# Kernel optimization log

Measured on AMD Instinct MI355X. Metric: run time of the kernel, lower is better.

## Reference

```python
import jax, jax.numpy as jnp
import numpy as np

D = 128
EPS = 1e-5

def group_norm1(x, gamma, beta):
    # GroupNorm with num_groups=1 over channel dim of [N, C]
    mu = jnp.mean(x, axis=-1, keepdims=True)
    var = jnp.mean(jnp.square(x - mu), axis=-1, keepdims=True)
    xhat = (x - mu) * jax.lax.rsqrt(var + EPS)
    return xhat * gamma + beta

def setup_inputs() -> dict:
    key = jax.random.key(0)
    ks = jax.random.split(key, 12)
    N_ctx, N_tgt, E = 40000, 40000, 640000
    s = 0.09  # ~1/sqrt(128) weight scale
    inp = {
        'context_feat': jax.random.normal(ks[0], (N_ctx, D), jnp.float32),
        'target_feat': jax.random.normal(ks[1], (N_tgt, D), jnp.float32),
        'context_pose': jax.random.normal(ks[2], (N_ctx, 4), jnp.float32),
        'target_pose': jax.random.normal(ks[3], (N_tgt, 4), jnp.float32),
        'W_input': s * jax.random.normal(ks[4], (D, D), jnp.float32),
        'W_rp': 0.5 * jax.random.normal(ks[5], (4, D), jnp.float32),
        'b_rp': jnp.zeros((D,), jnp.float32),
        'W_c1': s * jax.random.normal(ks[6], (2 * D, D), jnp.float32),
        'g_c1': jnp.ones((D,), jnp.float32),
        'b_c1': jnp.zeros((D,), jnp.float32),
        'W_c2': s * jax.random.normal(ks[7], (D, D), jnp.float32),
        'g_n': jnp.ones((D,), jnp.float32),
        'b_n': jnp.zeros((D,), jnp.float32),
        'W_m1': s * jax.random.normal(ks[8], (D, D), jnp.float32),
        'g_m1': jnp.ones((D,), jnp.float32),
        'bm1': jnp.zeros((D,), jnp.float32),
        'W_m2': s * jax.random.normal(ks[9], (D, D), jnp.float32),
        'g_m2': jnp.ones((D,), jnp.float32),
        'bm2': jnp.zeros((D,), jnp.float32),
        'hi': jax.random.randint(ks[10], (E,), 0, N_ctx, jnp.int32),
        'wi': jax.random.randint(ks[11], (E,), 0, N_tgt, jnp.int32),
    }
    return inp

def reference(context_feat, target_feat, context_pose, target_pose,
              W_input, W_rp, b_rp, W_c1, g_c1, b_c1, W_c2,
              g_n, b_n, W_m1, g_m1, bm1, W_m2, g_m2, bm2, hi, wi):
    # relpose: Linear(4,128) + ReLU on relative pose of each (context, target) edge
    dist_feat = context_pose[hi] - target_pose[wi]                 # [E, 4]
    dist_feat = jax.nn.relu(dist_feat @ W_rp + b_rp)               # [E, 128]
    # ctx: Linear(256,128,GN,ReLU) -> Linear(128,128, no bias)
    ctx = jnp.concatenate([context_feat[hi], dist_feat], axis=-1)  # [E, 256]
    ctx = jax.nn.relu(group_norm1(ctx @ W_c1, g_c1, b_c1))
    ctx = ctx @ W_c2                                               # [E, 128]
    # input linear + index_add scatter into targets
    tf = target_feat @ W_input                                     # [N_tgt, 128]
    tf = tf + jax.ops.segment_sum(ctx, wi, num_segments=target_feat.shape[0])
    tf = jax.nn.relu(group_norm1(tf, g_n, b_n))
    # mlp: Linear(GN,ReLU) -> Linear(GN, no act)
    tf = jax.nn.relu(group_norm1(tf @ W_m1, g_m1, bm1))
    tf = group_norm1(tf @ W_m2, g_m2, bm2)
    # residual + relu
    return jax.nn.relu(tf + target_feat)
```

## Files before the change

kernel.cpp:

```cpp
#include <hip/hip_runtime.h>

#define D 128
#define EPSV 1e-5f

typedef __attribute__((ext_vector_type(8))) __bf16 bf16x8;
typedef __attribute__((ext_vector_type(4))) float f32x4;

__device__ __forceinline__ ushort f2bf(float x) {
  unsigned u = __float_as_uint(x);
  u += 0x7fffu + ((u >> 16) & 1u);
  return (ushort)(u >> 16);
}
__device__ __forceinline__ unsigned cvtpk(float lo, float hi) {
  unsigned r;
  asm("v_cvt_pk_bf16_f32 %0, %1, %2" : "=v"(r) : "v"(lo), "v"(hi));
  return r;
}
__device__ __forceinline__ int yidx(int row, int col) {
  return row * 128 + (col ^ ((row & 7) << 3));
}

__global__ void k_cvt(const float* __restrict__ Wc1, const float* __restrict__ Wc2,
                      ushort* __restrict__ WT1, ushort* __restrict__ WT2) {
  int i = blockIdx.x * 256 + threadIdx.x;
  if (i < 128 * 256) {
    int n = i >> 8, k = i & 255;
    WT1[i] = f2bf(Wc1[k * 128 + n]);
  } else {
    int j = i - 128 * 256;
    if (j < 128 * 128) {
      int n = j >> 7, k = j & 127;
      WT2[j] = f2bf(Wc2[k * 128 + n]);
    }
  }
}

__global__ void k_cvtf(const float* __restrict__ cf, ushort* __restrict__ cb,
                       int n8) {
  int i = blockIdx.x * 256 + threadIdx.x;
  if (i < n8) {
    float4 f0 = *(const float4*)(cf + (size_t)i * 8);
    float4 f1 = *(const float4*)(cf + (size_t)i * 8 + 4);
    uint4 p;
    p.x = cvtpk(f0.x, f0.y); p.y = cvtpk(f0.z, f0.w);
    p.z = cvtpk(f1.x, f1.y); p.w = cvtpk(f1.z, f1.w);
    *(uint4*)(cb + (size_t)i * 8) = p;
  }
}

template <bool BF16CF>
__global__ __launch_bounds__(256, 3) void k_edge(
    const float* __restrict__ cfeat, const ushort* __restrict__ cfb,
    const float* __restrict__ cpose, const float* __restrict__ tpose,
    const float* __restrict__ Wrp, const float* __restrict__ brp,
    const float* __restrict__ gc1, const float* __restrict__ bc1,
    const ushort* __restrict__ WT1, const ushort* __restrict__ WT2,
    const int* __restrict__ hi, const int* __restrict__ wi,
    float* __restrict__ acc, int E) {
  __shared__ ushort Wbuf[2][4096];
  __shared__ ushort Ybuf[128 * 128];
  __shared__ float gnbuf[2][128][2];
  __shared__ int wl[128];

  const int t = threadIdx.x;
  const int lane = t & 63;
  const int wv = t >> 6;
  const int wm = wv >> 1, wn = wv & 1;
  const int s = lane & 15, g = lane >> 4;
  const int e0 = blockIdx.x * 128;

  auto stage = [&](int c, int nb) {
    const ushort* Wt = (c < 8) ? WT1 : WT2;
    const int koff = (c < 8 ? c : c - 8) * 32;
    const int krow = (c < 8) ? 256 : 128;
    const int col = t & 127, g0 = t >> 7;
#pragma unroll
    for (int v = 0; v < 2; ++v) {
      const int gg = g0 + v * 2;
      const ushort* src = Wt + (size_t)col * krow + koff + gg * 8;
      ushort* dst = &Wbuf[nb][(gg * 128 + col) * 8];
      __builtin_amdgcn_global_load_lds(
          (const __attribute__((address_space(1))) void*)src,
          (__attribute__((address_space(3))) void*)dst, 16, 0, 0);
    }
  };

  stage(0, 0);
  if (t < 128) wl[t] = wi[min(e0 + t, E - 1)];

  int hl[4];
#pragma unroll
  for (int m = 0; m < 4; ++m)
    hl[m] = hi[min(e0 + wm * 64 + m * 16 + s, E - 1)];

  bf16x8 cf01[2][4];
  if (BF16CF) {
#pragma unroll
    for (int kc = 0; kc < 2; ++kc)
#pragma unroll
      for (int m = 0; m < 4; ++m)
        cf01[kc][m] =
            *(const bf16x8*)(cfb + (size_t)hl[m] * D + kc * 32 + g * 8);
  }

  {
    const int e = t >> 1;
    const int jh = (t & 1) * 64;
    const int ge = min(e0 + e, E - 1);
    const int h = hi[ge], w = wi[ge];
    float4 cp = *(const float4*)(cpose + (size_t)h * 4);
    float4 tp = *(const float4*)(tpose + (size_t)w * 4);
    const float d0 = cp.x - tp.x, d1 = cp.y - tp.y;
    const float d2 = cp.z - tp.z, d3 = cp.w - tp.w;
#pragma unroll
    for (int q = 0; q < 16; ++q) {
      const int j = jh + q * 4;
      float4 b  = *(const float4*)(brp + j);
      float4 w0 = *(const float4*)(Wrp + j);
      float4 w1 = *(const float4*)(Wrp + D + j);
      float4 w2 = *(const float4*)(Wrp + 2 * D + j);
      float4 w3 = *(const float4*)(Wrp + 3 * D + j);
      float r0 = fmaxf(b.x + d0 * w0.x + d1 * w1.x + d2 * w2.x + d3 * w3.x, 0.f);
      float r1 = fmaxf(b.y + d0 * w0.y + d1 * w1.y + d2 * w2.y + d3 * w3.y, 0.f);
      float r2 = fmaxf(b.z + d0 * w0.z + d1 * w1.z + d2 * w2.z + d3 * w3.z, 0.f);
      float r3 = fmaxf(b.w + d0 * w0.w + d1 * w1.w + d2 * w2.w + d3 * w3.w, 0.f);
      *(uint2*)&Ybuf[yidx(e, j)] = make_uint2(cvtpk(r0, r1), cvtpk(r2, r3));
    }
  }
  __syncthreads();

  f32x4 acc1[4][4];
#pragma unroll
  for (int m = 0; m < 4; ++m)
#pragma unroll
    for (int n = 0; n < 4; ++n) acc1[m][n] = (f32x4){0.f, 0.f, 0.f, 0.f};

  for (int kc = 0; kc < 8; ++kc) {
    const int nb = kc & 1;
    stage(kc + 1, nb ^ 1);
    bf16x8 a[4];
    if (kc < 4) {
      if (BF16CF) {
        if (kc < 2) {
#pragma unroll
          for (int m = 0; m < 4; ++m) a[m] = cf01[kc][m];
        } else {
#pragma unroll
          for (int m = 0; m < 4; ++m)
            a[m] = *(const bf16x8*)(cfb + (size_t)hl[m] * D + kc * 32 + g * 8);
        }
      } else {
#pragma unroll
        for (int m = 0; m < 4; ++m) {
          const float* src = cfeat + (size_t)hl[m] * D + kc * 32 + g * 8;
          float4 f0 = *(const float4*)src;
          float4 f1 = *(const float4*)(src + 4);
          union { uint4 u; bf16x8 v; } cv;
          cv.u.x = cvtpk(f0.x, f0.y); cv.u.y = cvtpk(f0.z, f0.w);
          cv.u.z = cvtpk(f1.x, f1.y); cv.u.w = cvtpk(f1.z, f1.w);
          a[m] = cv.v;
        }
      }
    } else {
#pragma unroll
      for (int m = 0; m < 4; ++m)
        a[m] = *(const bf16x8*)
            &Ybuf[yidx(wm * 64 + m * 16 + s, (kc - 4) * 32 + g * 8)];
    }
#pragma unroll
    for (int n = 0; n < 4; ++n) {
      bf16x8 b = *(const bf16x8*)
          &Wbuf[nb][(g * 128 + wn * 64 + n * 16 + s) * 8];
#pragma unroll
      for (int m = 0; m < 4; ++m)
        acc1[m][n] =
            __builtin_amdgcn_mfma_f32_16x16x32_bf16(a[m], b, acc1[m][n], 0, 0, 0);
    }
    __syncthreads();
  }

#pragma unroll
  for (int m = 0; m < 4; ++m) {
#pragma unroll
    for (int reg = 0; reg < 4; ++reg) {
      float p1 = acc1[m][0][reg] + acc1[m][1][reg] + acc1[m][2][reg] +
                 acc1[m][3][reg];
      float p2 = acc1[m][0][reg] * acc1[m][0][reg] +
                 acc1[m][1][reg] * acc1[m][1][reg] +
                 acc1[m][2][reg] * acc1[m][2][reg] +
                 acc1[m][3][reg] * acc1[m][3][reg];
#pragma unroll
      for (int msk = 1; msk < 16; msk <<= 1) {
        p1 += __shfl_xor(p1, msk, 64);
        p2 += __shfl_xor(p2, msk, 64);
      }
      if (s == 0) {
        const int row = wm * 64 + m * 16 + g * 4 + reg;
        *(float2*)&gnbuf[wn][row][0] = make_float2(p1, p2);
      }
    }
  }
  __syncthreads();

  {
    float gcl[4], bcl[4];
#pragma unroll
    for (int n = 0; n < 4; ++n) {
      gcl[n] = gc1[wn * 64 + n * 16 + s];
      bcl[n] = bc1[wn * 64 + n * 16 + s];
    }
#pragma unroll
    for (int m = 0; m < 4; ++m) {
#pragma unroll
      for (int reg = 0; reg < 4; ++reg) {
        const int row = wm * 64 + m * 16 + g * 4 + reg;
        float2 q0 = *(const float2*)&gnbuf[0][row][0];
        float2 q1 = *(const float2*)&gnbuf[1][row][0];
        const float mean = (q0.x + q1.x) * (1.f / 128.f);
        const float var = (q0.y + q1.y) * (1.f / 128.f) - mean * mean;
        const float rstd = rsqrtf(var + EPSV);
#pragma unroll
        for (int n = 0; n < 4; ++n) {
          float y = fmaxf((acc1[m][n][reg] - mean) * rstd * gcl[n] + bcl[n], 0.f);
          Ybuf[yidx(row, wn * 64 + n * 16 + s)] = (ushort)cvtpk(y, y);
        }
      }
    }
  }
  __syncthreads();

  f32x4 acc2[4][4];
#pragma unroll
  for (int m = 0; m < 4; ++m)
#pragma unroll
    for (int n = 0; n < 4; ++n) acc2[m][n] = (f32x4){0.f, 0.f, 0.f, 0.f};

  for (int kc = 0; kc < 4; ++kc) {
    const int c = 8 + kc;
    const int nb = c & 1;
    if (c < 11) stage(c + 1, nb ^ 1);
    bf16x8 a[4];
#pragma unroll
    for (int m = 0; m < 4; ++m)
      a[m] = *(const bf16x8*)
          &Ybuf[yidx(wm * 64 + m * 16 + s, kc * 32 + g * 8)];
#pragma unroll
    for (int n = 0; n < 4; ++n) {
      bf16x8 b = *(const bf16x8*)
          &Wbuf[nb][(g * 128 + wn * 64 + n * 16 + s) * 8];
#pragma unroll
      for (int m = 0; m < 4; ++m)
        acc2[m][n] =
            __builtin_amdgcn_mfma_f32_16x16x32_bf16(a[m], b, acc2[m][n], 0, 0, 0);
    }
    if (kc < 3) __syncthreads();
  }

#pragma unroll
  for (int m = 0; m < 4; ++m) {
#pragma unroll
    for (int reg = 0; reg < 4; ++reg) {
      const int rl = wm * 64 + m * 16 + g * 4 + reg;
      if (e0 + rl < E) {
        const int w = wl[rl];
        float* base = acc + (size_t)w * D + wn * 64 + s;
#pragma unroll
        for (int n = 0; n < 4; ++n)
          unsafeAtomicAdd(base + n * 16, acc2[m][n][reg]);
      }
    }
  }
}

__device__ __forceinline__ void reduce16(float& a, float& b) {
#pragma unroll
  for (int w = 1; w < 16; w <<= 1) {
    a += __shfl_xor(a, w, 64);
    b += __shfl_xor(b, w, 64);
  }
}

__global__ __launch_bounds__(256, 2) void k_input(
    const float* __restrict__ tfeat, const float* __restrict__ Wi,
    float* __restrict__ acc, int N) {
  __shared__ float Wbuf[64][132];
  __shared__ float xt[64][132];
  const int t = threadIdx.x;
  const int r = t >> 4, s = t & 15, j0 = s * 8;
  const int row0 = blockIdx.x * 64;

  for (int idx = t; idx < 64 * 32; idx += 256) {
    int rr = idx >> 5, c4 = idx & 31;
    int grow = row0 + rr;
    float4 v = make_float4(0.f, 0.f, 0.f, 0.f);
    if (grow < N) v = *(const float4*)(tfeat + (size_t)grow * D + c4 * 4);
    *(float4*)&xt[rr][c4 * 4] = v;
  }

  float a[4][8] = {};
  for (int kc = 0; kc < 2; ++kc) {
    __syncthreads();
    for (int idx = t; idx < 64 * 32; idx += 256) {
      int kk = idx >> 5, c4 = idx & 31;
      *(float4*)&Wbuf[kk][c4 * 4] =
          *(const float4*)(Wi + (size_t)(kc * 64 + kk) * D + c4 * 4);
    }
    __syncthreads();
#pragma unroll 4
    for (int kk = 0; kk < 64; ++kk) {
      float4 w0 = *(const float4*)&Wbuf[kk][j0];
      float4 w1 = *(const float4*)&Wbuf[kk][j0 + 4];
#pragma unroll
      for (int i = 0; i < 4; ++i) {
        float xv = xt[r + 16 * i][kc * 64 + kk];
        a[i][0] += xv * w0.x; a[i][1] += xv * w0.y;
        a[i][2] += xv * w0.z; a[i][3] += xv * w0.w;
        a[i][4] += xv * w1.x; a[i][5] += xv * w1.y;
        a[i][6] += xv * w1.z; a[i][7] += xv * w1.w;
      }
    }
  }
#pragma unroll
  for (int i = 0; i < 4; ++i) {
    int row = row0 + r + 16 * i;
    if (row < N) {
      *(float4*)(acc + (size_t)row * D + j0) =
          make_float4(a[i][0], a[i][1], a[i][2], a[i][3]);
      *(float4*)(acc + (size_t)row * D + j0 + 4) =
          make_float4(a[i][4], a[i][5], a[i][6], a[i][7]);
    }
  }
}

__global__ __launch_bounds__(256, 2) void k_node(
    const float* __restrict__ tfeat,
    const float* __restrict__ gn, const float* __restrict__ bn,
    const float* __restrict__ Wm1, const float* __restrict__ gm1,
    const float* __restrict__ bm1,
    const float* __restrict__ Wm2, const float* __restrict__ gm2,
    const float* __restrict__ bm2,
    float* __restrict__ acc, int N) {
  __shared__ float Wbuf[64][132];
  __shared__ float xt[64][132];
  const int t = threadIdx.x;
  const int r = t >> 4, s = t & 15, j0 = s * 8;
  const int row0 = blockIdx.x * 64;

  auto stageW = [&](const float* W, int kc) {
    for (int idx = t; idx < 64 * 32; idx += 256) {
      int kk = idx >> 5, c4 = idx & 31;
      *(float4*)&Wbuf[kk][c4 * 4] =
          *(const float4*)(W + (size_t)(kc * 64 + kk) * D + c4 * 4);
    }
  };
  auto gemm = [&](float (&a)[4][8], int kc) {
#pragma unroll 4
    for (int kk = 0; kk < 64; ++kk) {
      float4 w0 = *(const float4*)&Wbuf[kk][j0];
      float4 w1 = *(const float4*)&Wbuf[kk][j0 + 4];
#pragma unroll
      for (int i = 0; i < 4; ++i) {
        float xv = xt[r + 16 * i][kc * 64 + kk];
        a[i][0] += xv * w0.x; a[i][1] += xv * w0.y;
        a[i][2] += xv * w0.z; a[i][3] += xv * w0.w;
        a[i][4] += xv * w1.x; a[i][5] += xv * w1.y;
        a[i][6] += xv * w1.z; a[i][7] += xv * w1.w;
      }
    }
  };

  {
    float gv[8], bv[8];
#pragma unroll
    for (int m = 0; m < 8; ++m) { gv[m] = gn[j0 + m]; bv[m] = bn[j0 + m]; }
#pragma unroll
    for (int i = 0; i < 4; ++i) {
      int row = row0 + r + 16 * i;
      float v[8] = {};
      if (row < N) {
        float4 v0 = *(const float4*)(acc + (size_t)row * D + j0);
        float4 v1 = *(const float4*)(acc + (size_t)row * D + j0 + 4);
        v[0] = v0.x; v[1] = v0.y; v[2] = v0.z; v[3] = v0.w;
        v[4] = v1.x; v[5] = v1.y; v[6] = v1.z; v[7] = v1.w;
      }
      float s1 = 0.f, s2 = 0.f;
#pragma unroll
      for (int m = 0; m < 8; ++m) { s1 += v[m]; s2 += v[m] * v[m]; }
      reduce16(s1, s2);
      float mean = s1 * (1.f / 128.f);
      float var = s2 * (1.f / 128.f) - mean * mean;
      float rstd = rsqrtf(var + EPSV);
#pragma unroll
      for (int m = 0; m < 8; ++m)
        xt[r + 16 * i][j0 + m] = fmaxf((v[m] - mean) * rstd * gv[m] + bv[m], 0.f);
    }
  }

  float a[4][8] = {};
  for (int kc = 0; kc < 2; ++kc) {
    __syncthreads();
    stageW(Wm1, kc);
    __syncthreads();
    gemm(a, kc);
  }
  __syncthreads();
  {
    float gv[8], bv[8];
#pragma unroll
    for (int m = 0; m < 8; ++m) { gv[m] = gm1[j0 + m]; bv[m] = bm1[j0 + m]; }
#pragma unroll
    for (int i = 0; i < 4; ++i) {
      float s1 = 0.f, s2 = 0.f;
#pragma unroll
      for (int m = 0; m < 8; ++m) { s1 += a[i][m]; s2 += a[i][m] * a[i][m]; }
      reduce16(s1, s2);
      float mean = s1 * (1.f / 128.f);
      float var = s2 * (1.f / 128.f) - mean * mean;
      float rstd = rsqrtf(var + EPSV);
#pragma unroll
      for (int m = 0; m < 8; ++m)
        xt[r + 16 * i][j0 + m] =
            fmaxf((a[i][m] - mean) * rstd * gv[m] + bv[m], 0.f);
    }
  }

  float a2[4][8] = {};
  for (int kc = 0; kc < 2; ++kc) {
    __syncthreads();
    stageW(Wm2, kc);
    __syncthreads();
    gemm(a2, kc);
  }
  {
    float gv[8], bv[8];
#pragma unroll
    for (int m = 0; m < 8; ++m) { gv[m] = gm2[j0 + m]; bv[m] = bm2[j0 + m]; }
#pragma unroll
    for (int i = 0; i < 4; ++i) {
      int row = row0 + r + 16 * i;
      float s1 = 0.f, s2 = 0.f;
#pragma unroll
      for (int m = 0; m < 8; ++m) { s1 += a2[i][m]; s2 += a2[i][m] * a2[i][m]; }
      reduce16(s1, s2);
      float mean = s1 * (1.f / 128.f);
      float var = s2 * (1.f / 128.f) - mean * mean;
      float rstd = rsqrtf(var + EPSV);
      if (row < N) {
        float o[8];
#pragma unroll
        for (int m = 0; m < 8; ++m) {
          float x = (a2[i][m] - mean) * rstd * gv[m] + bv[m];
          o[m] = fmaxf(x + tfeat[(size_t)row * D + j0 + m], 0.f);
        }
        *(float4*)(acc + (size_t)row * D + j0) =
            make_float4(o[0], o[1], o[2], o[3]);
        *(float4*)(acc + (size_t)row * D + j0 + 4) =
            make_float4(o[4], o[5], o[6], o[7]);
      }
    }
  }
}

extern "C" void kernel_launch(void* const* d_in, const int* in_sizes, int n_in,
                              void* d_out, int out_size, void* d_ws,
                              size_t ws_size, hipStream_t stream) {
  const float* cfeat = (const float*)d_in[0];
  const float* tfeat = (const float*)d_in[1];
  const float* cpose = (const float*)d_in[2];
  const float* tpose = (const float*)d_in[3];
  const float* Wi    = (const float*)d_in[4];
  const float* Wrp   = (const float*)d_in[5];
  const float* brp   = (const float*)d_in[6];
  const float* Wc1   = (const float*)d_in[7];
  const float* gc1   = (const float*)d_in[8];
  const float* bc1   = (const float*)d_in[9];
  const float* Wc2   = (const float*)d_in[10];
  const float* gn    = (const float*)d_in[11];
  const float* bn    = (const float*)d_in[12];
  const float* Wm1   = (const float*)d_in[13];
  const float* gm1   = (const float*)d_in[14];
  const float* bm1   = (const float*)d_in[15];
  const float* Wm2   = (const float*)d_in[16];
  const float* gm2   = (const float*)d_in[17];
  const float* bm2   = (const float*)d_in[18];
  const int* hi      = (const int*)d_in[19];
  const int* wi      = (const int*)d_in[20];

  const int N = in_sizes[1] / D;
  const int E = in_sizes[19];
  const int CFE = in_sizes[0];
  float* out = (float*)d_out;

  uint8_t* ws = (uint8_t*)d_ws;
  ushort* WT1 = (ushort*)ws;
  ushort* WT2 = (ushort*)(ws + 65536);
  ushort* cfb = (ushort*)(ws + 98304);
  const bool bf16cf = ws_size >= 98304 + (size_t)CFE * 2;

  const int nbN = (N + 63) / 64;
  const int nbE = (E + 127) / 128;

  k_cvt<<<192, 256, 0, stream>>>(Wc1, Wc2, WT1, WT2);
  if (bf16cf)
    k_cvtf<<<(CFE / 8 + 255) / 256, 256, 0, stream>>>(cfeat, cfb, CFE / 8);
  k_input<<<nbN, 256, 0, stream>>>(tfeat, Wi, out, N);
  if (bf16cf)
    k_edge<true><<<nbE, 256, 0, stream>>>(cfeat, cfb, cpose, tpose, Wrp, brp,
                                          gc1, bc1, WT1, WT2, hi, wi, out, E);
  else
    k_edge<false><<<nbE, 256, 0, stream>>>(cfeat, cfb, cpose, tpose, Wrp, brp,
                                           gc1, bc1, WT1, WT2, hi, wi, out, E);
  k_node<<<nbN, 256, 0, stream>>>(tfeat, gn, bn, Wm1, gm1, bm1, Wm2, gm2, bm2,
                                  out, N);
}
```

Baseline: 450.8 us.

## Fuse input linear into node kernel, scatter edges into separate zeroed buffer

When the workspace has room, edge messages are scattered into a separate memset-zeroed buffer S instead of the output. The target_feat @ W_input GEMM moves into the node kernel, which adds S before the first group norm. This drops the separate k_input launch and its write/read round trip of the output tensor. In exchange it adds a memset of S, extra workspace, and more work in k_node.

```diff
diff --git a/kernel.cpp b/kernel.cpp
--- a/kernel.cpp
+++ b/kernel.cpp
@@ -56,7 +56,7 @@
     const float* __restrict__ gc1, const float* __restrict__ bc1,
     const ushort* __restrict__ WT1, const ushort* __restrict__ WT2,
     const int* __restrict__ hi, const int* __restrict__ wi,
-    float* __restrict__ acc, int E) {
+    float* __restrict__ accS, int E) {
   __shared__ ushort Wbuf[2][4096];
   __shared__ ushort Ybuf[128 * 128];
   __shared__ float gnbuf[2][128][2];
@@ -263,7 +263,7 @@
       const int rl = wm * 64 + m * 16 + g * 4 + reg;
       if (e0 + rl < E) {
         const int w = wl[rl];
-        float* base = acc + (size_t)w * D + wn * 64 + s;
+        float* base = accS + (size_t)w * D + wn * 64 + s;
 #pragma unroll
         for (int n = 0; n < 4; ++n)
           unsafeAtomicAdd(base + n * 16, acc2[m][n][reg]);
@@ -332,8 +332,10 @@
   }
 }
 
+template <bool FUSE>
 __global__ __launch_bounds__(256, 2) void k_node(
-    const float* __restrict__ tfeat,
+    const float* __restrict__ tfeat, const float* __restrict__ S,
+    const float* __restrict__ Wi,
     const float* __restrict__ gn, const float* __restrict__ bn,
     const float* __restrict__ Wm1, const float* __restrict__ gm1,
     const float* __restrict__ bm1,
@@ -368,46 +370,10 @@
       }
     }
   };
-
-  {
+  auto gnorm = [&](float (&a)[4][8], const float* gv_, const float* bv_) {
     float gv[8], bv[8];
 #pragma unroll
-    for (int m = 0; m < 8; ++m) { gv[m] = gn[j0 + m]; bv[m] = bn[j0 + m]; }
-#pragma unroll
-    for (int i = 0; i < 4; ++i) {
-      int row = row0 + r + 16 * i;
-      float v[8] = {};
-      if (row < N) {
-        float4 v0 = *(const float4*)(acc + (size_t)row * D + j0);
-        float4 v1 = *(const float4*)(acc + (size_t)row * D + j0 + 4);
-        v[0] = v0.x; v[1] = v0.y; v[2] = v0.z; v[3] = v0.w;
-        v[4] = v1.x; v[5] = v1.y; v[6] = v1.z; v[7] = v1.w;
-      }
-      float s1 = 0.f, s2 = 0.f;
-#pragma unroll
-      for (int m = 0; m < 8; ++m) { s1 += v[m]; s2 += v[m] * v[m]; }
-      reduce16(s1, s2);
-      float mean = s1 * (1.f / 128.f);
-      float var = s2 * (1.f / 128.f) - mean * mean;
-      float rstd = rsqrtf(var + EPSV);
-#pragma unroll
-      for (int m = 0; m < 8; ++m)
-        xt[r + 16 * i][j0 + m] = fmaxf((v[m] - mean) * rstd * gv[m] + bv[m], 0.f);
-    }
-  }
-
-  float a[4][8] = {};
-  for (int kc = 0; kc < 2; ++kc) {
-    __syncthreads();
-    stageW(Wm1, kc);
-    __syncthreads();
-    gemm(a, kc);
-  }
-  __syncthreads();
-  {
-    float gv[8], bv[8];
-#pragma unroll
-    for (int m = 0; m < 8; ++m) { gv[m] = gm1[j0 + m]; bv[m] = bm1[j0 + m]; }
+    for (int m = 0; m < 8; ++m) { gv[m] = gv_[j0 + m]; bv[m] = bv_[j0 + m]; }
 #pragma unroll
     for (int i = 0; i < 4; ++i) {
       float s1 = 0.f, s2 = 0.f;
@@ -422,7 +388,57 @@
         xt[r + 16 * i][j0 + m] =
             fmaxf((a[i][m] - mean) * rstd * gv[m] + bv[m], 0.f);
     }
-  }
+  };
+
+  float a0[4][8] = {};
+  if (FUSE) {
+    for (int idx = t; idx < 64 * 32; idx += 256) {
+      int rr = idx >> 5, c4 = idx & 31;
+      int grow = row0 + rr;
+      float4 v = make_float4(0.f, 0.f, 0.f, 0.f);
+      if (grow < N) v = *(const float4*)(tfeat + (size_t)grow * D + c4 * 4);
+      *(float4*)&xt[rr][c4 * 4] = v;
+    }
+    for (int kc = 0; kc < 2; ++kc) {
+      __syncthreads();
+      stageW(Wi, kc);
+      __syncthreads();
+      gemm(a0, kc);
+    }
+#pragma unroll
+    for (int i = 0; i < 4; ++i) {
+      int row = row0 + r + 16 * i;
+      if (row < N) {
+        float4 v0 = *(const float4*)(S + (size_t)row * D + j0);
+        float4 v1 = *(const float4*)(S + (size_t)row * D + j0 + 4);
+        a0[i][0] += v0.x; a0[i][1] += v0.y; a0[i][2] += v0.z; a0[i][3] += v0.w;
+        a0[i][4] += v1.x; a0[i][5] += v1.y; a0[i][6] += v1.z; a0[i][7] += v1.w;
+      }
+    }
+    __syncthreads();
+  } else {
+#pragma unroll
+    for (int i = 0; i < 4; ++i) {
+      int row = row0 + r + 16 * i;
+      if (row < N) {
+        float4 v0 = *(const float4*)(acc + (size_t)row * D + j0);
+        float4 v1 = *(const float4*)(acc + (size_t)row * D + j0 + 4);
+        a0[i][0] = v0.x; a0[i][1] = v0.y; a0[i][2] = v0.z; a0[i][3] = v0.w;
+        a0[i][4] = v1.x; a0[i][5] = v1.y; a0[i][6] = v1.z; a0[i][7] = v1.w;
+      }
+    }
+  }
+  gnorm(a0, gn, bn);
+
+  float a[4][8] = {};
+  for (int kc = 0; kc < 2; ++kc) {
+    __syncthreads();
+    stageW(Wm1, kc);
+    __syncthreads();
+    gemm(a, kc);
+  }
+  __syncthreads();
+  gnorm(a, gm1, bm1);
 
   float a2[4][8] = {};
   for (int kc = 0; kc < 2; ++kc) {
@@ -495,7 +511,13 @@
   ushort* WT1 = (ushort*)ws;
   ushort* WT2 = (ushort*)(ws + 65536);
   ushort* cfb = (ushort*)(ws + 98304);
-  const bool bf16cf = ws_size >= 98304 + (size_t)CFE * 2;
+  const size_t cfb_end = 98304 + (size_t)CFE * 2;
+  float* S = (float*)(ws + ((cfb_end + 255) & ~(size_t)255));
+  const size_t sBytes = (size_t)N * D * 4;
+  const size_t s_end = ((cfb_end + 255) & ~(size_t)255) + sBytes;
+
+  const bool bf16cf = ws_size >= cfb_end;
+  const bool fuse = bf16cf && (ws_size >= s_end);
 
   const int nbN = (N + 63) / 64;
   const int nbE = (E + 127) / 128;
@@ -503,13 +525,27 @@
   k_cvt<<<192, 256, 0, stream>>>(Wc1, Wc2, WT1, WT2);
   if (bf16cf)
     k_cvtf<<<(CFE / 8 + 255) / 256, 256, 0, stream>>>(cfeat, cfb, CFE / 8);
-  k_input<<<nbN, 256, 0, stream>>>(tfeat, Wi, out, N);
+
+  float* accS;
+  if (fuse) {
+    hipMemsetAsync(S, 0, sBytes, stream);
+    accS = S;
+  } else {
+    k_input<<<nbN, 256, 0, stream>>>(tfeat, Wi, out, N);
+    accS = out;
+  }
+
   if (bf16cf)
     k_edge<true><<<nbE, 256, 0, stream>>>(cfeat, cfb, cpose, tpose, Wrp, brp,
-                                          gc1, bc1, WT1, WT2, hi, wi, out, E);
+                                          gc1, bc1, WT1, WT2, hi, wi, accS, E);
   else
     k_edge<false><<<nbE, 256, 0, stream>>>(cfeat, cfb, cpose, tpose, Wrp, brp,
-                                           gc1, bc1, WT1, WT2, hi, wi, out, E);
-  k_node<<<nbN, 256, 0, stream>>>(tfeat, gn, bn, Wm1, gm1, bm1, Wm2, gm2, bm2,
-                                  out, N);
-}
+                                           gc1, bc1, WT1, WT2, hi, wi, accS, E);
+
+  if (fuse)
+    k_node<true><<<nbN, 256, 0, stream>>>(tfeat, S, Wi, gn, bn, Wm1, gm1, bm1,
+                                          Wm2, gm2, bm2, out, N);
+  else
+    k_node<false><<<nbN, 256, 0, stream>>>(tfeat, S, Wi, gn, bn, Wm1, gm1, bm1,
+                                           Wm2, gm2, bm2, out, N);
+}
```

Result: no change. 451.8 us (+0.2%).
